# Performance work log

Measured on AMD Instinct MI355X. Metric: run time of the kernel, lower is better.

Reference implementation:

```python
import jax, jax.numpy as jnp
import numpy as np

H_DIM = 1024
N_HEADS = 16
B, T = 2, 2048
NEG = -1e9


def setup_inputs() -> dict:
    key = jax.random.key(0)
    ks = jax.random.split(key, 5)
    s = 1.0 / np.sqrt(H_DIM)
    return {
        "x": jax.random.normal(ks[0], (B, T, H_DIM), dtype=jnp.float32),
        "W_qkv": jax.random.normal(ks[1], (H_DIM, 3 * H_DIM), dtype=jnp.float32) * s,
        "b_qkv": jnp.zeros((3 * H_DIM,), dtype=jnp.float32),
        "W_proj": jax.random.normal(ks[2], (H_DIM, H_DIM), dtype=jnp.float32) * s,
        "b_proj": jnp.zeros((H_DIM,), dtype=jnp.float32),
    }


def reference(x, W_qkv, b_qkv, W_proj, b_proj):
    Bsz, Tlen, C = x.shape
    N = N_HEADS
    D = C // N
    qkv = x @ W_qkv + b_qkv                      # [B,T,3C]
    q, k, v = jnp.split(qkv, 3, axis=-1)
    # [B,T,C] -> [B,N,T,D]
    def to_heads(t):
        return t.reshape(Bsz, Tlen, N, D).transpose(0, 2, 1, 3)
    q, k, v = to_heads(q), to_heads(k), to_heads(v)
    scores = jnp.einsum('bntd,bnsd->bnts', q, k) / jnp.sqrt(jnp.float32(D))
    # additive mask exactly as original: (1 - tril) * -1e9
    mask = jnp.tril(jnp.ones((Tlen, Tlen), dtype=scores.dtype))
    scores = scores + (1.0 - mask) * NEG
    probs = jax.nn.softmax(scores, axis=-1)
    attn = jnp.einsum('bnts,bnsd->bntd', probs, v)   # [B,N,T,D]
    attn = attn.transpose(0, 2, 1, 3).reshape(Bsz, Tlen, C)
    return attn @ W_proj + b_proj
```

## Files before the change

### kernel.cpp

```cpp
#include <hip/hip_runtime.h>
#include <hip/hip_bf16.h>
#include <stdint.h>

typedef __attribute__((ext_vector_type(8))) short short8;
typedef __attribute__((ext_vector_type(4))) short s16x4;
typedef __attribute__((ext_vector_type(4))) float floatx4;
typedef __attribute__((ext_vector_type(4))) unsigned short ushortx4;

#define T_LEN 2048
#define C_DIM 1024
#define NH 16
#define HD 64

static __device__ __forceinline__ unsigned short f2bf(float f) {
  union { float f; unsigned u; } v; v.f = f;
  unsigned r = v.u + 0x7fffu + ((v.u >> 16) & 1u);
  return (unsigned short)(r >> 16);
}

static __device__ __forceinline__ void stage16(const void* g, void* l) {
  __builtin_amdgcn_global_load_lds(
      (const __attribute__((address_space(1))) void*)g,
      (__attribute__((address_space(3))) void*)l, 16, 0, 0);
}

static __device__ __forceinline__ floatx4 mfma16(s16x4 a, s16x4 b, floatx4 c) {
  asm("v_mfma_f32_16x16x16_bf16 %0, %1, %2, %0" : "+v"(c) : "v"(a), "v"(b));
  return c;
}
static __device__ __forceinline__ unsigned cvt_pk_bf16(float lo, float hi) {
  unsigned r;
  asm("v_cvt_pk_bf16_f32 %0, %1, %2" : "=v"(r) : "v"(lo), "v"(hi));
  return r;
}

static __device__ __forceinline__ void tc_body(
    const float* __restrict__ in, unsigned short* __restrict__ out,
    int R, int C, int bx, int by, int tid, unsigned short (*tile)[72]) {
  const int r0 = by * 64;
  const int c0 = bx * 64;
#pragma unroll
  for (int e = 0; e < 4; ++e) {
    const int ch = e * 256 + tid;
    const int r = ch >> 4, c4 = (ch & 15) * 4;
    const float4 v = *(const float4*)(in + (long)(r0 + r) * C + c0 + c4);
    tile[r][c4 + 0] = f2bf(v.x);
    tile[r][c4 + 1] = f2bf(v.y);
    tile[r][c4 + 2] = f2bf(v.z);
    tile[r][c4 + 3] = f2bf(v.w);
  }
  __syncthreads();
#pragma unroll
  for (int e = 0; e < 2; ++e) {
    const int ch = e * 256 + tid;
    const int c = ch >> 3, k8 = (ch & 7) * 8;
    short8 w;
#pragma unroll
    for (int j = 0; j < 8; ++j) w[j] = (short)tile[k8 + j][c];
    *(short8*)(out + (long)(c0 + c) * R + r0 + k8) = w;
  }
}

__global__ __launch_bounds__(256) void prep(
    const float* __restrict__ x, unsigned short* __restrict__ xbf,
    const float* __restrict__ Wqkv, unsigned short* __restrict__ Wqkvt,
    const float* __restrict__ Wproj, unsigned short* __restrict__ Wprojt) {
  __shared__ unsigned short tile[64][72];
  const int bid = (int)blockIdx.x;
  const int tid = (int)threadIdx.x;
  if (bid < 4096) {
    const long i = ((long)bid * 256 + tid) * 4;
    const float4 v = *(const float4*)(x + i);
    ushortx4 o;
    o[0] = f2bf(v.x); o[1] = f2bf(v.y); o[2] = f2bf(v.z); o[3] = f2bf(v.w);
    *(ushortx4*)(xbf + i) = o;
  } else if (bid < 4096 + 768) {
    const int t = bid - 4096;
    tc_body(Wqkv, Wqkvt, 1024, 3072, t % 48, t / 48, tid, tile);
  } else {
    const int t = bid - 4864;
    tc_body(Wproj, Wprojt, 1024, 1024, t % 16, t / 16, tid, tile);
  }
}

#define GSTAGE(BUF, K0) do {                                                          \
    _Pragma("unroll") for (int r = 0; r < 2; ++r) {                                   \
      const int ch = r * 256 + tid;                                                   \
      const int trow = ch >> 2, tcol = (ch & 3) * 8;                                  \
      stage16(Abase + (long)trow * K + (K0) + tcol, &As[BUF][(r * 256 + wid * 64) * 8]); \
      stage16(Bbase + (long)trow * K + (K0) + tcol, &Bs[BUF][(r * 256 + wid * 64) * 8]); \
    } } while (0)

template <int MODE>
__global__ __launch_bounds__(256) void gemm_bt(
    const unsigned short* __restrict__ A,
    const unsigned short* __restrict__ Bt,
    const float* __restrict__ bias,
    int M, int N, int K, int nbx,
    unsigned short* __restrict__ q_out,
    unsigned short* __restrict__ k_out,
    unsigned short* __restrict__ v_out,
    float* __restrict__ f_out) {
  __shared__ unsigned short As[2][128 * 32];
  __shared__ unsigned short Bs[2][128 * 32];
  const int tid = threadIdx.x;
  const int lane = tid & 63;
  const int wid = tid >> 6;
  const int wr = wid >> 1, wc = wid & 1;
  const int lrow = lane & 15, lgrp = lane >> 4;
  const int bid = (int)blockIdx.x;
  const int v = (bid & 7) * ((int)gridDim.x >> 3) + (bid >> 3);
  const long row0 = (long)(v / nbx) * 128;
  const long col0 = (long)(v % nbx) * 128;

  floatx4 acc[4][4];
#pragma unroll
  for (int m = 0; m < 4; ++m)
#pragma unroll
    for (int n = 0; n < 4; ++n)
      acc[m][n] = (floatx4){0.f, 0.f, 0.f, 0.f};

  const unsigned short* Abase = A + row0 * K;
  const unsigned short* Bbase = Bt + col0 * K;
  const int NT = K >> 5;

  GSTAGE(0, 0);
  asm volatile("s_waitcnt vmcnt(0)" ::: "memory");
  __builtin_amdgcn_s_barrier();

  int cur = 0;
  for (int t = 0; t < NT - 1; ++t) {
    GSTAGE(cur ^ 1, (t + 1) * 32);
    short8 af[4], bf[4];
#pragma unroll
    for (int m = 0; m < 4; ++m)
      af[m] = *(const short8*)&As[cur][(wr * 64 + m * 16 + lrow) * 32 + lgrp * 8];
#pragma unroll
    for (int n = 0; n < 4; ++n)
      bf[n] = *(const short8*)&Bs[cur][(wc * 64 + n * 16 + lrow) * 32 + lgrp * 8];
    __builtin_amdgcn_s_setprio(1);
#pragma unroll
    for (int m = 0; m < 4; ++m)
#pragma unroll
      for (int n = 0; n < 4; ++n)
        acc[m][n] = __builtin_amdgcn_mfma_f32_16x16x32_bf16(af[m], bf[n], acc[m][n], 0, 0, 0);
    __builtin_amdgcn_s_setprio(0);
    asm volatile("s_waitcnt vmcnt(0)" ::: "memory");
    __builtin_amdgcn_s_barrier();
    cur ^= 1;
  }
  {
    short8 af[4], bf[4];
#pragma unroll
    for (int m = 0; m < 4; ++m)
      af[m] = *(const short8*)&As[cur][(wr * 64 + m * 16 + lrow) * 32 + lgrp * 8];
#pragma unroll
    for (int n = 0; n < 4; ++n)
      bf[n] = *(const short8*)&Bs[cur][(wc * 64 + n * 16 + lrow) * 32 + lgrp * 8];
#pragma unroll
    for (int m = 0; m < 4; ++m)
#pragma unroll
      for (int n = 0; n < 4; ++n)
        acc[m][n] = __builtin_amdgcn_mfma_f32_16x16x32_bf16(af[m], bf[n], acc[m][n], 0, 0, 0);
  }

  if (MODE == 0) {
#pragma unroll
    for (int n = 0; n < 4; ++n) {
      const int c = (int)col0 + wc * 64 + n * 16 + lrow;
      const float bs = bias[c];
      const int sect = c >> 10;
      const int h = (c & 1023) >> 6;
      const int d = c & 63;
      const float scl = sect == 0 ? 0.18033688011112042f : 1.0f;
#pragma unroll
      for (int m = 0; m < 4; ++m) {
#pragma unroll
        for (int i = 0; i < 4; ++i) {
          const long r = row0 + wr * 64 + m * 16 + lgrp * 4 + i;
          const long b = r >> 11;
          const long t = r & 2047;
          const float val = (acc[m][n][i] + bs) * scl;
          if (sect == 2) {
            v_out[((b * NH + h) * HD + d) * T_LEN + t] = f2bf(val);
          } else {
            unsigned short* dst = sect == 0 ? q_out : k_out;
            dst[((b * NH + h) * T_LEN + t) * HD + d] = f2bf(val);
          }
        }
      }
    }
  } else {
#pragma unroll
    for (int n = 0; n < 4; ++n) {
      const int c = (int)col0 + wc * 64 + n * 16 + lrow;
      const float bs = bias[c];
#pragma unroll
      for (int m = 0; m < 4; ++m) {
#pragma unroll
        for (int i = 0; i < 4; ++i) {
          const long r = row0 + wr * 64 + m * 16 + lgrp * 4 + i;
          f_out[r * (long)N + c] = acc[m][n][i] + bs;
        }
      }
    }
  }
}

__global__ __launch_bounds__(256) void attn_fwd(
    const unsigned short* __restrict__ Qb,
    const unsigned short* __restrict__ Kb,
    const unsigned short* __restrict__ Vt,
    unsigned short* __restrict__ attn) {
  __shared__ float osum[32][68];
  __shared__ float mshare[4][2][16];
  __shared__ float sshare[4][2][16];
  const int bid = (int)blockIdx.x;
  const int xcd = bid & 7;
  const int j = bid >> 3;
  const int bh = xcd * 4 + (j & 3);
  const int qt = 63 - (j >> 2);
  const int b = bh >> 4, h = bh & 15;
  const int wid = (int)threadIdx.x >> 6;
  const int lane = (int)threadIdx.x & 63;
  const int lrow = lane & 15, lgrp = lane >> 4;
  const int q0 = qt * 32;
  const int nsteps = (q0 + 32 + 63) >> 6;

  const unsigned short* Qh = Qb + (long)bh * T_LEN * HD;
  const unsigned short* Kh = Kb + (long)bh * T_LEN * HD;
  const unsigned short* Vh = Vt + (long)bh * HD * T_LEN;

  short8 aq[2][2];
#pragma unroll
  for (int qs = 0; qs < 2; ++qs)
#pragma unroll
    for (int kk = 0; kk < 2; ++kk)
      aq[qs][kk] = *(const short8*)(Qh + (long)(q0 + qs * 16 + lrow) * HD + kk * 32 + lgrp * 8);

  float m_i[2] = {-1e30f, -1e30f};
  float s_i[2] = {0.f, 0.f};
  floatx4 o[2][4];
#pragma unroll
  for (int qs = 0; qs < 2; ++qs)
#pragma unroll
    for (int d0 = 0; d0 < 4; ++d0) o[qs][d0] = (floatx4){0.f, 0.f, 0.f, 0.f};

  for (int st = wid; st < nsteps; st += 4) {
    const int s0 = st * 64;
    short8 kf[4][2];
#pragma unroll
    for (int sc = 0; sc < 4; ++sc)
#pragma unroll
      for (int kk = 0; kk < 2; ++kk)
        kf[sc][kk] = *(const short8*)(Kh + (long)(s0 + sc * 16 + lrow) * HD + kk * 32 + lgrp * 8);
    s16x4 vb[4][4];
#pragma unroll
    for (int d0 = 0; d0 < 4; ++d0)
#pragma unroll
      for (int sc = 0; sc < 4; ++sc)
        vb[d0][sc] = *(const s16x4*)(Vh + (long)(d0 * 16 + lrow) * T_LEN + s0 + sc * 16 + lgrp * 4);
    floatx4 sf[2][4];
#pragma unroll
    for (int qs = 0; qs < 2; ++qs)
#pragma unroll
      for (int sc = 0; sc < 4; ++sc) sf[qs][sc] = (floatx4){0.f, 0.f, 0.f, 0.f};
    __builtin_amdgcn_s_setprio(1);
#pragma unroll
    for (int sc = 0; sc < 4; ++sc) {
#pragma unroll
      for (int kk = 0; kk < 2; ++kk) {
        sf[0][sc] = __builtin_amdgcn_mfma_f32_16x16x32_bf16(kf[sc][kk], aq[0][kk], sf[0][sc], 0, 0, 0);
        sf[1][sc] = __builtin_amdgcn_mfma_f32_16x16x32_bf16(kf[sc][kk], aq[1][kk], sf[1][sc], 0, 0, 0);
      }
    }
    __builtin_amdgcn_s_setprio(0);
    if (s0 + 64 > q0) {
#pragma unroll
      for (int qs = 0; qs < 2; ++qs) {
        const int q = q0 + qs * 16 + lrow;
#pragma unroll
        for (int sc = 0; sc < 4; ++sc) {
#pragma unroll
          for (int i = 0; i < 4; ++i) {
            const int s = s0 + sc * 16 + lgrp * 4 + i;
            if (s > q) sf[qs][sc][i] = -1e30f;
          }
        }
      }
    }
    s16x4 pa[2][4];
#pragma unroll
    for (int qs = 0; qs < 2; ++qs) {
      float m0 = fmaxf(fmaxf(sf[qs][0][0], sf[qs][0][1]), fmaxf(sf[qs][0][2], sf[qs][0][3]));
      float m1 = fmaxf(fmaxf(sf[qs][1][0], sf[qs][1][1]), fmaxf(sf[qs][1][2], sf[qs][1][3]));
      float m2 = fmaxf(fmaxf(sf[qs][2][0], sf[qs][2][1]), fmaxf(sf[qs][2][2], sf[qs][2][3]));
      float m3 = fmaxf(fmaxf(sf[qs][3][0], sf[qs][3][1]), fmaxf(sf[qs][3][2], sf[qs][3][3]));
      float mm = fmaxf(fmaxf(m0, m1), fmaxf(m2, m3));
      mm = fmaxf(mm, __shfl_xor(mm, 16));
      mm = fmaxf(mm, __shfl_xor(mm, 32));
      const int grow = !__all(mm <= m_i[qs]);
      float scale = 1.0f;
      if (grow) {
        const float mnew = fmaxf(m_i[qs], mm);
        scale = exp2f(m_i[qs] - mnew);
        m_i[qs] = mnew;
      }
      float rs = 0.f;
#pragma unroll
      for (int sc = 0; sc < 4; ++sc) {
#pragma unroll
        for (int i = 0; i < 4; ++i) {
          const float pv = exp2f(sf[qs][sc][i] - m_i[qs]);
          sf[qs][sc][i] = pv;
          rs += pv;
        }
      }
      rs += __shfl_xor(rs, 16);
      rs += __shfl_xor(rs, 32);
      s_i[qs] = s_i[qs] * scale + rs;
      if (grow) {
#pragma unroll
        for (int i = 0; i < 4; ++i) {
          const float sbc = __shfl(scale, 4 * lgrp + i);
#pragma unroll
          for (int d0 = 0; d0 < 4; ++d0) o[qs][d0][i] *= sbc;
        }
      }
#pragma unroll
      for (int sc = 0; sc < 4; ++sc) {
        union { unsigned u[2]; s16x4 v; } tmp;
        tmp.u[0] = cvt_pk_bf16(sf[qs][sc][0], sf[qs][sc][1]);
        tmp.u[1] = cvt_pk_bf16(sf[qs][sc][2], sf[qs][sc][3]);
        pa[qs][sc] = tmp.v;
      }
    }
    __builtin_amdgcn_s_setprio(1);
#pragma unroll
    for (int d0 = 0; d0 < 4; ++d0) {
#pragma unroll
      for (int sc = 0; sc < 4; ++sc) {
        o[0][d0] = mfma16(pa[0][sc], vb[d0][sc], o[0][d0]);
        o[1][d0] = mfma16(pa[1][sc], vb[d0][sc], o[1][d0]);
      }
    }
    __builtin_amdgcn_s_setprio(0);
  }

  mshare[wid][0][lrow] = m_i[0];
  mshare[wid][1][lrow] = m_i[1];
  __syncthreads();
  float fb2[2][4];
#pragma unroll
  for (int qs = 0; qs < 2; ++qs) {
    const float gm = fmaxf(fmaxf(mshare[0][qs][lrow], mshare[1][qs][lrow]),
                           fmaxf(mshare[2][qs][lrow], mshare[3][qs][lrow]));
    const float f = exp2f(m_i[qs] - gm);
    sshare[wid][qs][lrow] = s_i[qs] * f;
#pragma unroll
    for (int i = 0; i < 4; ++i) fb2[qs][i] = __shfl(f, 4 * lgrp + i);
  }
#pragma unroll
  for (int w = 0; w < 4; ++w) {
    if (wid == w) {
#pragma unroll
      for (int qs = 0; qs < 2; ++qs) {
#pragma unroll
        for (int i = 0; i < 4; ++i) {
#pragma unroll
          for (int d0 = 0; d0 < 4; ++d0) {
            const int qq = qs * 16 + lgrp * 4 + i;
            const int dd = d0 * 16 + lrow;
            const float vv = o[qs][d0][i] * fb2[qs][i];
            if (w == 0) osum[qq][dd] = vv;
            else        osum[qq][dd] += vv;
          }
        }
      }
    }
    __syncthreads();
  }
  const int t = wid * 64 + lane;
  const int q = t >> 3;
  const int d8 = (t & 7) * 8;
  const int qss = q >> 4, qr = q & 15;
  const float S = sshare[0][qss][qr] + sshare[1][qss][qr] +
                  sshare[2][qss][qr] + sshare[3][qss][qr];
  const float invS = 1.0f / S;
  short8 wv;
#pragma unroll
  for (int jj = 0; jj < 8; ++jj)
    wv[jj] = (short)f2bf(osum[q][d8 + jj] * invS);
  *(short8*)(attn + (long)(b * T_LEN + q0 + q) * C_DIM + h * HD + d8) = wv;
}

extern "C" void kernel_launch(void* const* d_in, const int* in_sizes, int n_in,
                              void* d_out, int out_size, void* d_ws, size_t ws_size,
                              hipStream_t stream) {
  const float* x     = (const float*)d_in[0];
  const float* Wqkv  = (const float*)d_in[1];
  const float* bqkv  = (const float*)d_in[2];
  const float* Wproj = (const float*)d_in[3];
  const float* bproj = (const float*)d_in[4];
  float* out = (float*)d_out;
  char* ws = (char*)d_ws;
  const size_t MB = 1024 * 1024;
  unsigned short* Qb     = (unsigned short*)(ws + 0 * MB);
  unsigned short* Kb     = (unsigned short*)(ws + 8 * MB);
  unsigned short* Vt     = (unsigned short*)(ws + 24 * MB);
  unsigned short* attn   = (unsigned short*)(ws + 32 * MB);
  unsigned short* xbf    = (unsigned short*)(ws + 40 * MB);
  unsigned short* Wqkvt  = (unsigned short*)(ws + 48 * MB);
  unsigned short* Wprojt = (unsigned short*)(ws + 54 * MB);

  prep<<<5120, 256, 0, stream>>>(x, xbf, Wqkv, Wqkvt, Wproj, Wprojt);
  gemm_bt<0><<<768, 256, 0, stream>>>(xbf, Wqkvt, bqkv, 4096, 3072, 1024, 24,
                                      Qb, Kb, Vt, nullptr);
  attn_fwd<<<2048, 256, 0, stream>>>(Qb, Kb, Vt, attn);
  gemm_bt<1><<<256, 256, 0, stream>>>(attn, Wprojt, bproj, 4096, 1024, 1024, 8,
                                      nullptr, nullptr, nullptr, out);
}
```

Baseline: 245.1 us.

## Share K/V tiles in LDS across waves with double-buffered async staging

The attention kernel moves from split-KV per block (four waves sharing one 32-row query tile, merged through LDS) to four waves each owning their own 32-row query tile in a 128-row block. K and V tiles are staged once into swizzled, double-buffered LDS with global_load_lds, so each tile is read from global memory once per block instead of once per wave. The grid shrinks from 2048 to 512 blocks and the cross-wave softmax merge is removed. The cost is a barrier on every step and idle waves on the causal diagonal. The QKV GEMM epilogue also packs four V values into a single vector store.

```diff
diff --git a/kernel.cpp b/kernel.cpp
--- a/kernel.cpp
+++ b/kernel.cpp
@@ -175,17 +175,22 @@
       const float scl = sect == 0 ? 0.18033688011112042f : 1.0f;
 #pragma unroll
       for (int m = 0; m < 4; ++m) {
-#pragma unroll
-        for (int i = 0; i < 4; ++i) {
-          const long r = row0 + wr * 64 + m * 16 + lgrp * 4 + i;
-          const long b = r >> 11;
-          const long t = r & 2047;
-          const float val = (acc[m][n][i] + bs) * scl;
-          if (sect == 2) {
-            v_out[((b * NH + h) * HD + d) * T_LEN + t] = f2bf(val);
-          } else {
-            unsigned short* dst = sect == 0 ? q_out : k_out;
-            dst[((b * NH + h) * T_LEN + t) * HD + d] = f2bf(val);
+        if (sect == 2) {
+          const long r0m = row0 + wr * 64 + m * 16 + lgrp * 4;
+          const long b = r0m >> 11;
+          const long t0 = r0m & 2047;
+          ushortx4 pk;
+#pragma unroll
+          for (int i = 0; i < 4; ++i) pk[i] = f2bf(acc[m][n][i] + bs);
+          *(ushortx4*)&v_out[((b * NH + h) * HD + d) * T_LEN + t0] = pk;
+        } else {
+          unsigned short* dst = sect == 0 ? q_out : k_out;
+#pragma unroll
+          for (int i = 0; i < 4; ++i) {
+            const long r = row0 + wr * 64 + m * 16 + lgrp * 4 + i;
+            const long b = r >> 11;
+            const long t = r & 2047;
+            dst[((b * NH + h) * T_LEN + t) * HD + d] = f2bf((acc[m][n][i] + bs) * scl);
           }
         }
       }
@@ -212,25 +217,43 @@
     const unsigned short* __restrict__ Kb,
     const unsigned short* __restrict__ Vt,
     unsigned short* __restrict__ attn) {
-  __shared__ float osum[32][68];
-  __shared__ float mshare[4][2][16];
-  __shared__ float sshare[4][2][16];
+  __shared__ unsigned short Ks[2][4096];
+  __shared__ unsigned short Vs[2][4096];
   const int bid = (int)blockIdx.x;
   const int xcd = bid & 7;
   const int j = bid >> 3;
   const int bh = xcd * 4 + (j & 3);
-  const int qt = 63 - (j >> 2);
+  const int qblk = 15 - (j >> 2);
   const int b = bh >> 4, h = bh & 15;
-  const int wid = (int)threadIdx.x >> 6;
-  const int lane = (int)threadIdx.x & 63;
+  const int tid = (int)threadIdx.x;
+  const int wid = tid >> 6;
+  const int lane = tid & 63;
   const int lrow = lane & 15, lgrp = lane >> 4;
-  const int q0 = qt * 32;
-  const int nsteps = (q0 + 32 + 63) >> 6;
+  const int q0 = qblk * 128 + wid * 32;
+  const int myext = q0 + 32;
+  const int blksteps = (qblk * 128 + 128) >> 6;
 
   const unsigned short* Qh = Qb + (long)bh * T_LEN * HD;
   const unsigned short* Kh = Kb + (long)bh * T_LEN * HD;
   const unsigned short* Vh = Vt + (long)bh * HD * T_LEN;
 
+  int koff[2], voff[2];
+#pragma unroll
+  for (int jj = 0; jj < 2; ++jj) {
+    const int c = wid * 128 + jj * 64 + lane;
+    const int row = c >> 3;
+    const int cs = ((c & 7) ^ (row & 7)) * 8;
+    koff[jj] = row * HD + cs;
+    voff[jj] = row * T_LEN + cs;
+  }
+
+#define ASTAGE(BUF, S0) do {                                                         \
+    _Pragma("unroll") for (int jj = 0; jj < 2; ++jj)                                 \
+      stage16(Kh + (long)(S0) * HD + koff[jj], &Ks[BUF][(wid * 128 + jj * 64) * 8]); \
+    _Pragma("unroll") for (int jj = 0; jj < 2; ++jj)                                 \
+      stage16(Vh + (long)(S0) + voff[jj], &Vs[BUF][(wid * 128 + jj * 64) * 8]);      \
+  } while (0)
+
   short8 aq[2][2];
 #pragma unroll
   for (int qs = 0; qs < 2; ++qs)
@@ -246,152 +269,129 @@
 #pragma unroll
     for (int d0 = 0; d0 < 4; ++d0) o[qs][d0] = (floatx4){0.f, 0.f, 0.f, 0.f};
 
-  for (int st = wid; st < nsteps; st += 4) {
+  ASTAGE(0, 0);
+  asm volatile("s_waitcnt vmcnt(0)" ::: "memory");
+  __builtin_amdgcn_s_barrier();
+
+  int cur = 0;
+  for (int st = 0; st < blksteps; ++st) {
     const int s0 = st * 64;
-    short8 kf[4][2];
-#pragma unroll
-    for (int sc = 0; sc < 4; ++sc)
-#pragma unroll
-      for (int kk = 0; kk < 2; ++kk)
-        kf[sc][kk] = *(const short8*)(Kh + (long)(s0 + sc * 16 + lrow) * HD + kk * 32 + lgrp * 8);
-    s16x4 vb[4][4];
-#pragma unroll
-    for (int d0 = 0; d0 < 4; ++d0)
-#pragma unroll
-      for (int sc = 0; sc < 4; ++sc)
-        vb[d0][sc] = *(const s16x4*)(Vh + (long)(d0 * 16 + lrow) * T_LEN + s0 + sc * 16 + lgrp * 4);
-    floatx4 sf[2][4];
-#pragma unroll
-    for (int qs = 0; qs < 2; ++qs)
-#pragma unroll
-      for (int sc = 0; sc < 4; ++sc) sf[qs][sc] = (floatx4){0.f, 0.f, 0.f, 0.f};
-    __builtin_amdgcn_s_setprio(1);
-#pragma unroll
-    for (int sc = 0; sc < 4; ++sc) {
-#pragma unroll
-      for (int kk = 0; kk < 2; ++kk) {
-        sf[0][sc] = __builtin_amdgcn_mfma_f32_16x16x32_bf16(kf[sc][kk], aq[0][kk], sf[0][sc], 0, 0, 0);
-        sf[1][sc] = __builtin_amdgcn_mfma_f32_16x16x32_bf16(kf[sc][kk], aq[1][kk], sf[1][sc], 0, 0, 0);
-      }
+    if (st + 1 < blksteps) ASTAGE(cur ^ 1, s0 + 64);
+    if (s0 < myext) {
+      floatx4 sf[2][4];
+#pragma unroll
+      for (int qs = 0; qs < 2; ++qs)
+#pragma unroll
+        for (int sc = 0; sc < 4; ++sc) sf[qs][sc] = (floatx4){0.f, 0.f, 0.f, 0.f};
+      __builtin_amdgcn_s_setprio(1);
+#pragma unroll
+      for (int sc = 0; sc < 4; ++sc) {
+        const int row = sc * 16 + lrow;
+        const int rsw = row & 7;
+        const short8 k0 = *(const short8*)&Ks[cur][row * 64 + (lgrp ^ rsw) * 8];
+        const short8 k1 = *(const short8*)&Ks[cur][row * 64 + ((4 + lgrp) ^ rsw) * 8];
+        sf[0][sc] = __builtin_amdgcn_mfma_f32_16x16x32_bf16(k0, aq[0][0], sf[0][sc], 0, 0, 0);
+        sf[1][sc] = __builtin_amdgcn_mfma_f32_16x16x32_bf16(k0, aq[1][0], sf[1][sc], 0, 0, 0);
+        sf[0][sc] = __builtin_amdgcn_mfma_f32_16x16x32_bf16(k1, aq[0][1], sf[0][sc], 0, 0, 0);
+        sf[1][sc] = __builtin_amdgcn_mfma_f32_16x16x32_bf16(k1, aq[1][1], sf[1][sc], 0, 0, 0);
+      }
+      __builtin_amdgcn_s_setprio(0);
+      if (s0 + 64 > q0) {
+#pragma unroll
+        for (int qs = 0; qs < 2; ++qs) {
+          const int q = q0 + qs * 16 + lrow;
+#pragma unroll
+          for (int sc = 0; sc < 4; ++sc) {
+#pragma unroll
+            for (int i = 0; i < 4; ++i) {
+              const int s = s0 + sc * 16 + lgrp * 4 + i;
+              if (s > q) sf[qs][sc][i] = -1e30f;
+            }
+          }
+        }
+      }
+      s16x4 pa[2][4];
+#pragma unroll
+      for (int qs = 0; qs < 2; ++qs) {
+        float m0 = fmaxf(fmaxf(sf[qs][0][0], sf[qs][0][1]), fmaxf(sf[qs][0][2], sf[qs][0][3]));
+        float m1 = fmaxf(fmaxf(sf[qs][1][0], sf[qs][1][1]), fmaxf(sf[qs][1][2], sf[qs][1][3]));
+        float m2 = fmaxf(fmaxf(sf[qs][2][0], sf[qs][2][1]), fmaxf(sf[qs][2][2], sf[qs][2][3]));
+        float m3 = fmaxf(fmaxf(sf[qs][3][0], sf[qs][3][1]), fmaxf(sf[qs][3][2], sf[qs][3][3]));
+        float mm = fmaxf(fmaxf(m0, m1), fmaxf(m2, m3));
+        mm = fmaxf(mm, __shfl_xor(mm, 16));
+        mm = fmaxf(mm, __shfl_xor(mm, 32));
+        const int grow = !__all(mm <= m_i[qs]);
+        float scale = 1.0f;
+        if (grow) {
+          const float mnew = fmaxf(m_i[qs], mm);
+          scale = exp2f(m_i[qs] - mnew);
+          m_i[qs] = mnew;
+        }
+        float rs = 0.f;
+#pragma unroll
+        for (int sc = 0; sc < 4; ++sc) {
+#pragma unroll
+          for (int i = 0; i < 4; ++i) {
+            const float pv = exp2f(sf[qs][sc][i] - m_i[qs]);
+            sf[qs][sc][i] = pv;
+            rs += pv;
+          }
+        }
+        rs += __shfl_xor(rs, 16);
+        rs += __shfl_xor(rs, 32);
+        s_i[qs] = s_i[qs] * scale + rs;
+        if (grow) {
+#pragma unroll
+          for (int i = 0; i < 4; ++i) {
+            const float sbc = __shfl(scale, 4 * lgrp + i);
+#pragma unroll
+            for (int d0 = 0; d0 < 4; ++d0) o[qs][d0][i] *= sbc;
+          }
+        }
+#pragma unroll
+        for (int sc = 0; sc < 4; ++sc) {
+          union { unsigned u[2]; s16x4 v; } tmp;
+          tmp.u[0] = cvt_pk_bf16(sf[qs][sc][0], sf[qs][sc][1]);
+          tmp.u[1] = cvt_pk_bf16(sf[qs][sc][2], sf[qs][sc][3]);
+          pa[qs][sc] = tmp.v;
+        }
+      }
+      __builtin_amdgcn_s_setprio(1);
+#pragma unroll
+      for (int d0 = 0; d0 < 4; ++d0) {
+        const int d = d0 * 16 + lrow;
+        const int dsw = d & 7;
+#pragma unroll
+        for (int sc = 0; sc < 4; ++sc) {
+          const int g = sc * 2 + (lgrp >> 1);
+          const s16x4 vb = *(const s16x4*)&Vs[cur][d * 64 + ((g ^ dsw)) * 8 + (lgrp & 1) * 4];
+          o[0][d0] = mfma16(pa[0][sc], vb, o[0][d0]);
+          o[1][d0] = mfma16(pa[1][sc], vb, o[1][d0]);
+        }
+      }
+      __builtin_amdgcn_s_setprio(0);
     }
-    __builtin_amdgcn_s_setprio(0);
-    if (s0 + 64 > q0) {
-#pragma unroll
-      for (int qs = 0; qs < 2; ++qs) {
-        const int q = q0 + qs * 16 + lrow;
-#pragma unroll
-        for (int sc = 0; sc < 4; ++sc) {
-#pragma unroll
-          for (int i = 0; i < 4; ++i) {
-            const int s = s0 + sc * 16 + lgrp * 4 + i;
-            if (s > q) sf[qs][sc][i] = -1e30f;
-          }
-        }
+    asm volatile("s_waitcnt vmcnt(0)" ::: "memory");
+    __builtin_amdgcn_s_barrier();
+    cur ^= 1;
+  }
+#undef ASTAGE
+
+#pragma unroll
+  for (int qs = 0; qs < 2; ++qs) {
+    float inv[4];
+#pragma unroll
+    for (int i = 0; i < 4; ++i) inv[i] = 1.0f / __shfl(s_i[qs], 4 * lgrp + i);
+#pragma unroll
+    for (int d0 = 0; d0 < 4; ++d0) {
+#pragma unroll
+      for (int i = 0; i < 4; ++i) {
+        const int q = q0 + qs * 16 + lgrp * 4 + i;
+        attn[(long)(b * T_LEN + q) * C_DIM + h * HD + d0 * 16 + lrow] =
+            f2bf(o[qs][d0][i] * inv[i]);
       }
     }
-    s16x4 pa[2][4];
-#pragma unroll
-    for (int qs = 0; qs < 2; ++qs) {
-      float m0 = fmaxf(fmaxf(sf[qs][0][0], sf[qs][0][1]), fmaxf(sf[qs][0][2], sf[qs][0][3]));
-      float m1 = fmaxf(fmaxf(sf[qs][1][0], sf[qs][1][1]), fmaxf(sf[qs][1][2], sf[qs][1][3]));
-      float m2 = fmaxf(fmaxf(sf[qs][2][0], sf[qs][2][1]), fmaxf(sf[qs][2][2], sf[qs][2][3]));
-      float m3 = fmaxf(fmaxf(sf[qs][3][0], sf[qs][3][1]), fmaxf(sf[qs][3][2], sf[qs][3][3]));
-      float mm = fmaxf(fmaxf(m0, m1), fmaxf(m2, m3));
-      mm = fmaxf(mm, __shfl_xor(mm, 16));
-      mm = fmaxf(mm, __shfl_xor(mm, 32));
-      const int grow = !__all(mm <= m_i[qs]);
-      float scale = 1.0f;
-      if (grow) {
-        const float mnew = fmaxf(m_i[qs], mm);
-        scale = exp2f(m_i[qs] - mnew);
-        m_i[qs] = mnew;
-      }
-      float rs = 0.f;
-#pragma unroll
-      for (int sc = 0; sc < 4; ++sc) {
-#pragma unroll
-        for (int i = 0; i < 4; ++i) {
-          const float pv = exp2f(sf[qs][sc][i] - m_i[qs]);
-          sf[qs][sc][i] = pv;
-          rs += pv;
-        }
-      }
-      rs += __shfl_xor(rs, 16);
-      rs += __shfl_xor(rs, 32);
-      s_i[qs] = s_i[qs] * scale + rs;
-      if (grow) {
-#pragma unroll
-        for (int i = 0; i < 4; ++i) {
-          const float sbc = __shfl(scale, 4 * lgrp + i);
-#pragma unroll
-          for (int d0 = 0; d0 < 4; ++d0) o[qs][d0][i] *= sbc;
-        }
-      }
-#pragma unroll
-      for (int sc = 0; sc < 4; ++sc) {
-        union { unsigned u[2]; s16x4 v; } tmp;
-        tmp.u[0] = cvt_pk_bf16(sf[qs][sc][0], sf[qs][sc][1]);
-        tmp.u[1] = cvt_pk_bf16(sf[qs][sc][2], sf[qs][sc][3]);
-        pa[qs][sc] = tmp.v;
-      }
-    }
-    __builtin_amdgcn_s_setprio(1);
-#pragma unroll
-    for (int d0 = 0; d0 < 4; ++d0) {
-#pragma unroll
-      for (int sc = 0; sc < 4; ++sc) {
-        o[0][d0] = mfma16(pa[0][sc], vb[d0][sc], o[0][d0]);
-        o[1][d0] = mfma16(pa[1][sc], vb[d0][sc], o[1][d0]);
-      }
-    }
-    __builtin_amdgcn_s_setprio(0);
-  }
-
-  mshare[wid][0][lrow] = m_i[0];
-  mshare[wid][1][lrow] = m_i[1];
-  __syncthreads();
-  float fb2[2][4];
-#pragma unroll
-  for (int qs = 0; qs < 2; ++qs) {
-    const float gm = fmaxf(fmaxf(mshare[0][qs][lrow], mshare[1][qs][lrow]),
-                           fmaxf(mshare[2][qs][lrow], mshare[3][qs][lrow]));
-    const float f = exp2f(m_i[qs] - gm);
-    sshare[wid][qs][lrow] = s_i[qs] * f;
-#pragma unroll
-    for (int i = 0; i < 4; ++i) fb2[qs][i] = __shfl(f, 4 * lgrp + i);
-  }
-#pragma unroll
-  for (int w = 0; w < 4; ++w) {
-    if (wid == w) {
-#pragma unroll
-      for (int qs = 0; qs < 2; ++qs) {
-#pragma unroll
-        for (int i = 0; i < 4; ++i) {
-#pragma unroll
-          for (int d0 = 0; d0 < 4; ++d0) {
-            const int qq = qs * 16 + lgrp * 4 + i;
-            const int dd = d0 * 16 + lrow;
-            const float vv = o[qs][d0][i] * fb2[qs][i];
-            if (w == 0) osum[qq][dd] = vv;
-            else        osum[qq][dd] += vv;
-          }
-        }
-      }
-    }
-    __syncthreads();
-  }
-  const int t = wid * 64 + lane;
-  const int q = t >> 3;
-  const int d8 = (t & 7) * 8;
-  const int qss = q >> 4, qr = q & 15;
-  const float S = sshare[0][qss][qr] + sshare[1][qss][qr] +
-                  sshare[2][qss][qr] + sshare[3][qss][qr];
-  const float invS = 1.0f / S;
-  short8 wv;
-#pragma unroll
-  for (int jj = 0; jj < 8; ++jj)
-    wv[jj] = (short)f2bf(osum[q][d8 + jj] * invS);
-  *(short8*)(attn + (long)(b * T_LEN + q0 + q) * C_DIM + h * HD + d8) = wv;
+  }
 }
 
 extern "C" void kernel_launch(void* const* d_in, const int* in_sizes, int n_in,
@@ -416,7 +416,7 @@
   prep<<<5120, 256, 0, stream>>>(x, xbf, Wqkv, Wqkvt, Wproj, Wprojt);
   gemm_bt<0><<<768, 256, 0, stream>>>(xbf, Wqkvt, bqkv, 4096, 3072, 1024, 24,
                                       Qb, Kb, Vt, nullptr);
-  attn_fwd<<<2048, 256, 0, stream>>>(Qb, Kb, Vt, attn);
+  attn_fwd<<<512, 256, 0, stream>>>(Qb, Kb, Vt, attn);
   gemm_bt<1><<<256, 256, 0, stream>>>(attn, Wprojt, bproj, 4096, 1024, 1024, 8,
                                       nullptr, nullptr, nullptr, out);
 }
```

After: 217.0 us. 1.13x faster.
